# Kernel tuning notes

Hardware: AMD Instinct MI355X
Metric: run time of the kernel (lower is better)

Reference implementation:

```python
import jax, jax.numpy as jnp
from jax import lax
import numpy as np

GAMMA = 0.25  # bottleneck commitment-loss weight (bn.gamma)
B, Q, N = 8, 64, 8192
K = 512       # n_quant_vecs (codebook size)
C = 256       # n_classes (mu-law quantization levels)


def setup_inputs() -> dict:
    key = jax.random.key(0)
    k1, k2, k3, k4 = jax.random.split(key, 4)
    ze = jax.random.normal(k1, (B, Q, N), dtype=jnp.float32)
    emb = jax.random.normal(k2, (K, Q), dtype=jnp.float32)
    quant_pred = jax.random.normal(k3, (B, C, N), dtype=jnp.float32)
    target_wav = jax.random.randint(k4, (B, N), 0, C, dtype=jnp.int64)
    return {"ze": ze, "emb": emb, "quant_pred": quant_pred, "target_wav": target_wav}


def reference(ze, emb, quant_pred, target_wav):
    # --- VQ codebook nearest-neighbor squared L2 distance ---
    # Original materializes (B,K,Q,N) diff; we use the expansion
    # ||z-e||^2 = ||z||^2 + ||e||^2 - 2 z.e to avoid the huge intermediate.
    ze2 = jnp.sum(ze * ze, axis=1)                       # (B,N)
    emb2 = jnp.sum(emb * emb, axis=1)                    # (K,)
    dots = jnp.einsum('bqn,kq->bkn', ze, emb)            # (B,K,N)
    d = ze2[:, None, :] + emb2[None, :, None] - 2.0 * dots  # (B,K,N)
    kmin = jnp.argmin(lax.stop_gradient(d), axis=1)      # (B,N)
    e_sel = emb[kmin]                                    # (B,N,Q) selected codewords
    ze_t = jnp.transpose(ze, (0, 2, 1))                  # (B,N,Q)

    # l2 loss: sg(ze) vs emb  -> gradient flows to codebook only
    l2_loss = jnp.sum((lax.stop_gradient(ze_t) - e_sel) ** 2, axis=-1)       # (B,N)
    # commitment loss: bn.min_dist uses sg(emb) -> gradient flows to ze only
    com_loss = GAMMA * jnp.sum((ze_t - lax.stop_gradient(e_sel)) ** 2, axis=-1)  # (B,N)

    # --- reconstruction CE: log-softmax over class dim + gather target ---
    log_pred = jax.nn.log_softmax(quant_pred, axis=1)    # (B,C,N)
    lp_t = jnp.take_along_axis(log_pred, target_wav[:, None, :], axis=1)[:, 0, :]  # (B,N)
    rec_loss = -lp_t

    total_loss = rec_loss.sum() + l2_loss.sum() + com_loss.sum()
    return total_loss
```

## Files before the change

### kernel.cpp

```cpp
#include <hip/hip_runtime.h>
#include <math.h>

#define GAMMA 0.25f
constexpr int B_ = 8, Q_ = 64, N_ = 8192, K_ = 512, C_ = 256;

typedef __attribute__((ext_vector_type(8))) short bf16x8;
typedef __attribute__((ext_vector_type(4))) short short4v;
typedef __attribute__((ext_vector_type(4))) float f32x4;

static __device__ inline short f2bf(float x) {
    union { float f; unsigned u; } v; v.f = x;
    unsigned r = (v.u + 0x7fffu + ((v.u >> 16) & 1u)) >> 16;
    return (short)r;
}
static __device__ inline float bf2f(short h) {
    union { unsigned u; float f; } v; v.u = ((unsigned)(unsigned short)h) << 16;
    return v.f;
}

__global__ __launch_bounds__(256) void prep_kernel(const float* __restrict__ emb,
                                                   short* __restrict__ embB,
                                                   float* __restrict__ e2g)
{
    const int r = blockIdx.x * 256 + threadIdx.x;
    if (r >= K_) return;
    const float4* src = (const float4*)(emb + r * Q_);
    short4v* dst = (short4v*)(embB + r * Q_);
    float s = 0.f;
    #pragma unroll
    for (int i = 0; i < 16; ++i) {
        const float4 v = src[i];
        short4v h;
        h[0] = f2bf(v.x); h[1] = f2bf(v.y); h[2] = f2bf(v.z); h[3] = f2bf(v.w);
        dst[i] = h;
        #pragma unroll
        for (int j = 0; j < 4; ++j) { const float a = bf2f(h[j]); s = fmaf(a, a, s); }
    }
    e2g[r] = s;
}

__global__ __launch_bounds__(256) void ce_kernel(const float* __restrict__ qp,
                                                 const int* __restrict__ tgt,
                                                 float* __restrict__ cePart)
{
    __shared__ f32x4 parts[32];
    const int tid  = threadIdx.x;
    const int lane = tid & 63;
    const int w    = tid >> 6;
    const int g    = lane & 7;
    const int c0   = lane >> 3;

    const int base = blockIdx.x * 32;
    const int b    = base >> 13;
    const int n0   = base & (N_ - 1);
    const float* qpb = qp + (size_t)b * C_ * N_;
    const float* qpn = qpb + n0 + g * 4;
    const int cbase  = w * 64 + c0 * 8;

    float4 v[8];
    #pragma unroll
    for (int j = 0; j < 8; ++j)
        v[j] = *(const float4*)(qpn + (size_t)(cbase + j) * N_);

    float xts[4] = {0.f, 0.f, 0.f, 0.f};
    if ((w == 0) && (lane < 8)) {
        #pragma unroll
        for (int j = 0; j < 4; ++j) {
            const int t = tgt[base + lane * 4 + j];
            xts[j] = qpb[(size_t)t * N_ + n0 + lane * 4 + j];
        }
    }

    f32x4 acc = {0.f, 0.f, 0.f, 0.f};
    #pragma unroll
    for (int j = 0; j < 8; ++j) {
        acc[0] += __expf(v[j].x); acc[1] += __expf(v[j].y);
        acc[2] += __expf(v[j].z); acc[3] += __expf(v[j].w);
    }
    #pragma unroll
    for (int r = 0; r < 4; ++r) {
        acc[r] += __shfl_xor(acc[r], 8, 64);
        acc[r] += __shfl_xor(acc[r], 16, 64);
        acc[r] += __shfl_xor(acc[r], 32, 64);
    }
    if (c0 == 0) parts[w * 8 + g] = acc;
    __syncthreads();

    if (w == 0) {
        float loss = 0.f;
        if (lane < 8) {
            const f32x4 tot = (parts[lane] + parts[8 + lane]) +
                              (parts[16 + lane] + parts[24 + lane]);
            #pragma unroll
            for (int j = 0; j < 4; ++j) loss += __logf(tot[j]) - xts[j];
        }
        loss += __shfl_down(loss, 4, 64);
        loss += __shfl_down(loss, 2, 64);
        loss += __shfl_down(loss, 1, 64);
        if (lane == 0) cePart[blockIdx.x] = loss;
    }
}

__global__ __launch_bounds__(256) void vq_kernel(const float* __restrict__ ze,
                                                 const short* __restrict__ embB,
                                                 const float* __restrict__ e2g,
                                                 float* __restrict__ vqPart)
{
    __shared__ float smem[256];
    const int tid  = threadIdx.x;
    const int lane = tid & 63;
    const int w    = tid >> 6;
    const int n16  = lane & 15;
    const int quad = lane >> 4;

    const int base = blockIdx.x * 64;
    const int b    = base >> 13;
    const int n0   = base & (N_ - 1);
    const float* zb = ze + (size_t)b * Q_ * N_;

    bf16x8 afrag[4][2];
    float zsq = 0.f;
    #pragma unroll
    for (int u = 0; u < 4; ++u) {
        const int nn = n0 + u * 16 + n16;
        #pragma unroll
        for (int s = 0; s < 2; ++s) {
            #pragma unroll
            for (int j = 0; j < 8; ++j) {
                const int q = s * 32 + quad * 8 + j;
                const float x = zb[(size_t)q * N_ + nn];
                zsq = fmaf(x, x, zsq);
                afrag[u][s][j] = f2bf(-2.f * x);
            }
        }
    }

    const short* bb = embB + (w * 128 + n16) * Q_ + quad * 8;
    bf16x8 Bv[8][2];
    float  e2v[8];
    #pragma unroll
    for (int t = 0; t < 8; ++t) {
        Bv[t][0] = *(const bf16x8*)(bb + t * 16 * Q_);
        Bv[t][1] = *(const bf16x8*)(bb + t * 16 * Q_ + 32);
        e2v[t]   = e2g[w * 128 + t * 16 + n16];
    }

    f32x4 best[4];
    #pragma unroll
    for (int u = 0; u < 4; ++u) best[u] = (f32x4){1e30f, 1e30f, 1e30f, 1e30f};

    #pragma unroll
    for (int t = 0; t < 8; ++t) {
        const f32x4 ce2 = {e2v[t], e2v[t], e2v[t], e2v[t]};
        #pragma unroll
        for (int u = 0; u < 4; ++u) {
            f32x4 a = __builtin_amdgcn_mfma_f32_16x16x32_bf16(afrag[u][0], Bv[t][0], ce2, 0, 0, 0);
            a       = __builtin_amdgcn_mfma_f32_16x16x32_bf16(afrag[u][1], Bv[t][1], a,   0, 0, 0);
            #pragma unroll
            for (int r = 0; r < 4; ++r) best[u][r] = fminf(best[u][r], a[r]);
        }
    }

    #pragma unroll
    for (int m = 1; m < 16; m <<= 1) {
        #pragma unroll
        for (int u = 0; u < 4; ++u) {
            #pragma unroll
            for (int r = 0; r < 4; ++r)
                best[u][r] = fminf(best[u][r], __shfl_xor(best[u][r], m, 64));
        }
    }
    if (n16 == 0) {
        #pragma unroll
        for (int u = 0; u < 4; ++u) {
            #pragma unroll
            for (int r = 0; r < 4; ++r)
                smem[w * 64 + u * 16 + quad * 4 + r] = best[u][r];
        }
    }
    __syncthreads();

    if (w == 0) {
        const float mn = fminf(fminf(smem[lane], smem[64 + lane]),
                               fminf(smem[128 + lane], smem[192 + lane]));
        float val = 1.25f * (mn + zsq);
        #pragma unroll
        for (int off = 32; off > 0; off >>= 1) val += __shfl_down(val, off, 64);
        if (lane == 0) vqPart[blockIdx.x] = val;
    }
}

__global__ __launch_bounds__(256) void reduce_kernel(const float* __restrict__ cePart,
                                                     const float* __restrict__ vqPart,
                                                     float* __restrict__ out)
{
    __shared__ float sm[4];
    const int tid = threadIdx.x;
    float s = 0.f;
    #pragma unroll
    for (int i = 0; i < 8; ++i) s += cePart[tid + i * 256];
    #pragma unroll
    for (int i = 0; i < 4; ++i) s += vqPart[tid + i * 256];
    #pragma unroll
    for (int off = 32; off > 0; off >>= 1) s += __shfl_down(s, off, 64);
    if ((tid & 63) == 0) sm[tid >> 6] = s;
    __syncthreads();
    if (tid == 0) out[0] = (sm[0] + sm[1]) + (sm[2] + sm[3]);
}

extern "C" void kernel_launch(void* const* d_in, const int* in_sizes, int n_in,
                              void* d_out, int out_size, void* d_ws, size_t ws_size,
                              hipStream_t stream) {
    const float* ze  = (const float*)d_in[0];
    const float* emb = (const float*)d_in[1];
    const float* qp  = (const float*)d_in[2];
    const int*   tgt = (const int*)d_in[3];
    float* out = (float*)d_out;

    short* embB   = (short*)d_ws;
    float* e2g    = (float*)((char*)d_ws + 65536);
    float* cePart = (float*)((char*)d_ws + 65536 + 2048);
    float* vqPart = (float*)((char*)d_ws + 65536 + 2048 + 8192);

    ce_kernel<<<2048, 256, 0, stream>>>(qp, tgt, cePart);
    prep_kernel<<<2, 256, 0, stream>>>(emb, embB, e2g);
    vq_kernel<<<1024, 256, 0, stream>>>(ze, embB, e2g, vqPart);
    reduce_kernel<<<1, 256, 0, stream>>>(cePart, vqPart, out);
}
```

Before: 132.3 us.

## Restructure CE kernel to 512-thread blocks covering 256 columns each

The cross-entropy kernel moves from 2048 blocks of 256 threads, each covering 32 columns, to 256 blocks of 512 threads, each covering 256 columns. Every lane now owns 4 contiguous columns, and each of 8 waves sums exp over 32 classes with 32 float4 loads issued up front. Partial sums go through shared memory, so the per-lane shuffle reduction goes away. The aim is more memory-level parallelism per thread and fewer blocks, at the risk of higher register pressure and only 256 blocks to fill the GPU.

```diff
diff --git a/kernel.cpp b/kernel.cpp
--- a/kernel.cpp
+++ b/kernel.cpp
@@ -39,31 +39,23 @@
     e2g[r] = s;
 }
 
-__global__ __launch_bounds__(256) void ce_kernel(const float* __restrict__ qp,
-                                                 const int* __restrict__ tgt,
-                                                 float* __restrict__ cePart)
-{
-    __shared__ f32x4 parts[32];
+__global__ void ce_kernel(const float* __restrict__ qp,
+                          const int* __restrict__ tgt,
+                          float* __restrict__ cePart)
+{
+    __shared__ f32x4 parts[8][64];
     const int tid  = threadIdx.x;
     const int lane = tid & 63;
     const int w    = tid >> 6;
-    const int g    = lane & 7;
-    const int c0   = lane >> 3;
-
-    const int base = blockIdx.x * 32;
+
+    const int base = blockIdx.x * 256;
     const int b    = base >> 13;
     const int n0   = base & (N_ - 1);
     const float* qpb = qp + (size_t)b * C_ * N_;
-    const float* qpn = qpb + n0 + g * 4;
-    const int cbase  = w * 64 + c0 * 8;
-
-    float4 v[8];
-    #pragma unroll
-    for (int j = 0; j < 8; ++j)
-        v[j] = *(const float4*)(qpn + (size_t)(cbase + j) * N_);
+    const float* qpn = qpb + n0 + lane * 4;
 
     float xts[4] = {0.f, 0.f, 0.f, 0.f};
-    if ((w == 0) && (lane < 8)) {
+    if (w == 0) {
         #pragma unroll
         for (int j = 0; j < 4; ++j) {
             const int t = tgt[base + lane * 4 + j];
@@ -72,31 +64,38 @@
     }
 
     f32x4 acc = {0.f, 0.f, 0.f, 0.f};
-    #pragma unroll
-    for (int j = 0; j < 8; ++j) {
-        acc[0] += __expf(v[j].x); acc[1] += __expf(v[j].y);
-        acc[2] += __expf(v[j].z); acc[3] += __expf(v[j].w);
-    }
-    #pragma unroll
-    for (int r = 0; r < 4; ++r) {
-        acc[r] += __shfl_xor(acc[r], 8, 64);
-        acc[r] += __shfl_xor(acc[r], 16, 64);
-        acc[r] += __shfl_xor(acc[r], 32, 64);
-    }
-    if (c0 == 0) parts[w * 8 + g] = acc;
+    const int cw = w * 32;
+    float4 v0[16], v1[16];
+    #pragma unroll
+    for (int j = 0; j < 16; ++j)
+        v0[j] = *(const float4*)(qpn + (size_t)(cw + j) * N_);
+    #pragma unroll
+    for (int j = 0; j < 16; ++j)
+        v1[j] = *(const float4*)(qpn + (size_t)(cw + 16 + j) * N_);
+    #pragma unroll
+    for (int j = 0; j < 16; ++j) {
+        acc[0] += __expf(v0[j].x); acc[1] += __expf(v0[j].y);
+        acc[2] += __expf(v0[j].z); acc[3] += __expf(v0[j].w);
+    }
+    #pragma unroll
+    for (int j = 0; j < 16; ++j) {
+        acc[0] += __expf(v1[j].x); acc[1] += __expf(v1[j].y);
+        acc[2] += __expf(v1[j].z); acc[3] += __expf(v1[j].w);
+    }
+
+    parts[w][lane] = acc;
     __syncthreads();
 
     if (w == 0) {
+        f32x4 tot = ((parts[0][lane] + parts[1][lane]) +
+                     (parts[2][lane] + parts[3][lane])) +
+                    ((parts[4][lane] + parts[5][lane]) +
+                     (parts[6][lane] + parts[7][lane]));
         float loss = 0.f;
-        if (lane < 8) {
-            const f32x4 tot = (parts[lane] + parts[8 + lane]) +
-                              (parts[16 + lane] + parts[24 + lane]);
-            #pragma unroll
-            for (int j = 0; j < 4; ++j) loss += __logf(tot[j]) - xts[j];
-        }
-        loss += __shfl_down(loss, 4, 64);
-        loss += __shfl_down(loss, 2, 64);
-        loss += __shfl_down(loss, 1, 64);
+        #pragma unroll
+        for (int j = 0; j < 4; ++j) loss += __logf(tot[j]) - xts[j];
+        #pragma unroll
+        for (int off = 32; off > 0; off >>= 1) loss += __shfl_down(loss, off, 64);
         if (lane == 0) cePart[blockIdx.x] = loss;
     }
 }
@@ -196,9 +195,7 @@
 {
     __shared__ float sm[4];
     const int tid = threadIdx.x;
-    float s = 0.f;
-    #pragma unroll
-    for (int i = 0; i < 8; ++i) s += cePart[tid + i * 256];
+    float s = cePart[tid];
     #pragma unroll
     for (int i = 0; i < 4; ++i) s += vqPart[tid + i * 256];
     #pragma unroll
@@ -220,9 +217,9 @@
     short* embB   = (short*)d_ws;
     float* e2g    = (float*)((char*)d_ws + 65536);
     float* cePart = (float*)((char*)d_ws + 65536 + 2048);
-    float* vqPart = (float*)((char*)d_ws + 65536 + 2048 + 8192);
-
-    ce_kernel<<<2048, 256, 0, stream>>>(qp, tgt, cePart);
+    float* vqPart = (float*)((char*)d_ws + 65536 + 2048 + 1024);
+
+    ce_kernel<<<256, 512, 0, stream>>>(qp, tgt, cePart);
     prep_kernel<<<2, 256, 0, stream>>>(emb, embB, e2g);
     vq_kernel<<<1024, 256, 0, stream>>>(ze, embB, e2g, vqPart);
     reduce_kernel<<<1, 256, 0, stream>>>(cePart, vqPart, out);
```

New measurement: 136.1 us. 2.9% more time.

## Split cross-entropy into contiguous streaming partial-sum pass plus finish kernel

Applied to the files above, without the earlier changes.

Replaces the per-column CE kernel, which read strided class rows, with a streaming kernel. Each block reads one contiguous 256KB slab of 32 class rows and writes partial exp-sums to an 8MB workspace. A finish kernel sums the 32 partials per position, takes the log and subtracts the target logit. This aims for fully sequential DRAM reads of the 64MB quant_pred. In exchange it adds 8MB of partial writes and reads, an extra launch, and a fallback path used when the workspace is too small.

```diff
diff --git a/kernel.cpp b/kernel.cpp
--- a/kernel.cpp
+++ b/kernel.cpp
@@ -39,9 +39,67 @@
     e2g[r] = s;
 }
 
-__global__ __launch_bounds__(256) void ce_kernel(const float* __restrict__ qp,
-                                                 const int* __restrict__ tgt,
-                                                 float* __restrict__ cePart)
+__global__ __launch_bounds__(512) void ce_stream_kernel(const float* __restrict__ qp,
+                                                        float* __restrict__ part)
+{
+    const int t   = threadIdx.x;
+    const int blk = blockIdx.x;
+    const float* src = qp + (size_t)blk * 65536 + t * 4;
+
+    f32x4 acc[4];
+    #pragma unroll
+    for (int j = 0; j < 4; ++j) acc[j] = (f32x4){0.f, 0.f, 0.f, 0.f};
+
+    #pragma unroll
+    for (int s = 0; s < 32; ++s) {
+        const float4 v = *(const float4*)(src + s * 2048);
+        acc[s & 3][0] += __expf(v.x);
+        acc[s & 3][1] += __expf(v.y);
+        acc[s & 3][2] += __expf(v.z);
+        acc[s & 3][3] += __expf(v.w);
+    }
+
+    float* dst = part + (size_t)blk * 8192 + t * 4;
+    *(f32x4*)(dst +    0) = acc[0];
+    *(f32x4*)(dst + 2048) = acc[1];
+    *(f32x4*)(dst + 4096) = acc[2];
+    *(f32x4*)(dst + 6144) = acc[3];
+}
+
+__global__ __launch_bounds__(256) void ce_finish_kernel(const float* __restrict__ qp,
+                                                        const float* __restrict__ part,
+                                                        const int* __restrict__ tgt,
+                                                        float* __restrict__ cePart)
+{
+    __shared__ float sm[4];
+    const int tid = threadIdx.x;
+    const int G   = blockIdx.x * 256 + tid;
+    const int b   = G >> 11;
+    const int n   = (G & 2047) * 4;
+
+    const float* p = part + (size_t)b * 32 * 8192 + n;
+    f32x4 s = {0.f, 0.f, 0.f, 0.f};
+    #pragma unroll
+    for (int k = 0; k < 32; ++k)
+        s += *(const f32x4*)(p + (size_t)k * 8192);
+
+    const float* qpb = qp + (size_t)b * C_ * N_;
+    float loss = 0.f;
+    #pragma unroll
+    for (int j = 0; j < 4; ++j) {
+        const int tg = tgt[b * N_ + n + j];
+        loss += __logf(s[j]) - qpb[(size_t)tg * N_ + n + j];
+    }
+    #pragma unroll
+    for (int off = 32; off > 0; off >>= 1) loss += __shfl_down(loss, off, 64);
+    if ((tid & 63) == 0) sm[tid >> 6] = loss;
+    __syncthreads();
+    if (tid == 0) cePart[blockIdx.x] = (sm[0] + sm[1]) + (sm[2] + sm[3]);
+}
+
+__global__ __launch_bounds__(256) void ce_fallback_kernel(const float* __restrict__ qp,
+                                                          const int* __restrict__ tgt,
+                                                          float* __restrict__ cePart)
 {
     __shared__ f32x4 parts[32];
     const int tid  = threadIdx.x;
@@ -191,14 +249,14 @@
 }
 
 __global__ __launch_bounds__(256) void reduce_kernel(const float* __restrict__ cePart,
+                                                     int ceN,
                                                      const float* __restrict__ vqPart,
                                                      float* __restrict__ out)
 {
     __shared__ float sm[4];
     const int tid = threadIdx.x;
     float s = 0.f;
-    #pragma unroll
-    for (int i = 0; i < 8; ++i) s += cePart[tid + i * 256];
+    for (int i = tid; i < ceN; i += 256) s += cePart[i];
     #pragma unroll
     for (int i = 0; i < 4; ++i) s += vqPart[tid + i * 256];
     #pragma unroll
@@ -219,11 +277,22 @@
 
     short* embB   = (short*)d_ws;
     float* e2g    = (float*)((char*)d_ws + 65536);
-    float* cePart = (float*)((char*)d_ws + 65536 + 2048);
-    float* vqPart = (float*)((char*)d_ws + 65536 + 2048 + 8192);
-
-    ce_kernel<<<2048, 256, 0, stream>>>(qp, tgt, cePart);
-    prep_kernel<<<2, 256, 0, stream>>>(emb, embB, e2g);
-    vq_kernel<<<1024, 256, 0, stream>>>(ze, embB, e2g, vqPart);
-    reduce_kernel<<<1, 256, 0, stream>>>(cePart, vqPart, out);
-}
+    float* vqPart = (float*)((char*)d_ws + 67584);
+    float* cePart = (float*)((char*)d_ws + 71680);
+    float* part   = (float*)((char*)d_ws + 79872);
+
+    const size_t need_stream = 79872 + (size_t)256 * 8192 * 4;
+
+    if (ws_size >= need_stream) {
+        ce_stream_kernel<<<256, 512, 0, stream>>>(qp, part);
+        prep_kernel<<<2, 256, 0, stream>>>(emb, embB, e2g);
+        vq_kernel<<<1024, 256, 0, stream>>>(ze, embB, e2g, vqPart);
+        ce_finish_kernel<<<64, 256, 0, stream>>>(qp, part, tgt, cePart);
+        reduce_kernel<<<1, 256, 0, stream>>>(cePart, 64, vqPart, out);
+    } else {
+        ce_fallback_kernel<<<2048, 256, 0, stream>>>(qp, tgt, cePart);
+        prep_kernel<<<2, 256, 0, stream>>>(emb, embB, e2g);
+        vq_kernel<<<1024, 256, 0, stream>>>(ze, embB, e2g, vqPart);
+        reduce_kernel<<<1, 256, 0, stream>>>(cePart, 2048, vqPart, out);
+    }
+}
```

After: 142.5 us. 7.7% more time.
